# Optimization experiments

Measured on AMD Instinct MI355X. Metric: run time of the kernel, lower is better.

The kernel has to match this reference:

```python
import jax, jax.numpy as jnp
import numpy as np
from jax import lax

DW_THR = 4.0
PW_THR = 1e-3
EPS = 1e-5


def _bn(x, gamma, beta, mean, var):
    # inference-mode BatchNorm2d over channel axis 1
    inv = gamma * lax.rsqrt(var + EPS)
    return x * inv[None, :, None, None] + (beta - mean * inv)[None, :, None, None]


def _prune(x, thr):
    # zero each (batch, channel) feature map whose max-abs < thr
    maxabs = jnp.max(jnp.abs(x), axis=(2, 3), keepdims=True)  # [B,C,1,1]
    return jnp.where(maxabs < thr, jnp.zeros((), x.dtype), x)


def setup_inputs() -> dict:
    key = jax.random.key(0)
    ks = jax.random.split(key, 8)
    B, Cin, Cout, H, W = 32, 256, 512, 56, 56
    x = jax.random.normal(ks[0], (B, Cin, H, W), jnp.float32)
    dw_w = jax.random.normal(ks[1], (Cin, 1, 3, 3), jnp.float32) * (1.0 / 3.0)
    dw_b = jax.random.normal(ks[2], (Cin,), jnp.float32) * 0.1
    bn1_gamma = jnp.ones((Cin,), jnp.float32)
    bn1_beta = jnp.zeros((Cin,), jnp.float32)
    bn1_mean = jnp.zeros((Cin,), jnp.float32)
    bn1_var = jnp.ones((Cin,), jnp.float32)
    pw_w = jax.random.normal(ks[3], (Cout, Cin), jnp.float32) * (1.0 / np.sqrt(Cin))
    pw_b = jax.random.normal(ks[4], (Cout,), jnp.float32) * 0.1
    bn2_gamma = jnp.ones((Cout,), jnp.float32)
    bn2_beta = jnp.zeros((Cout,), jnp.float32)
    bn2_mean = jnp.zeros((Cout,), jnp.float32)
    bn2_var = jnp.ones((Cout,), jnp.float32)
    return dict(x=x, dw_w=dw_w, dw_b=dw_b,
                bn1_gamma=bn1_gamma, bn1_beta=bn1_beta, bn1_mean=bn1_mean, bn1_var=bn1_var,
                pw_w=pw_w, pw_b=pw_b,
                bn2_gamma=bn2_gamma, bn2_beta=bn2_beta, bn2_mean=bn2_mean, bn2_var=bn2_var)


def reference(x, dw_w, dw_b, bn1_gamma, bn1_beta, bn1_mean, bn1_var,
              pw_w, pw_b, bn2_gamma, bn2_beta, bn2_mean, bn2_var):
    Cin = x.shape[1]
    # depthwise 3x3 conv, padding=1, groups=Cin
    y = lax.conv_general_dilated(
        x, dw_w, window_strides=(1, 1), padding=((1, 1), (1, 1)),
        feature_group_count=Cin,
        dimension_numbers=('NCHW', 'OIHW', 'NCHW'))
    y = y + dw_b[None, :, None, None]
    y = jax.nn.relu(_bn(y, bn1_gamma, bn1_beta, bn1_mean, bn1_var))
    y = _prune(y, DW_THR)
    # pointwise 1x1 conv == channel GEMM
    z = jnp.einsum('bchw,oc->bohw', y, pw_w) + pw_b[None, :, None, None]
    z = jax.nn.relu(_bn(z, bn2_gamma, bn2_beta, bn2_mean, bn2_var))
    z = _prune(z, PW_THR)
    return z
```

## Files before the change

kernel.cpp:

```cpp
#include <hip/hip_runtime.h>
#include <hip/hip_bf16.h>

#define EPSV 1e-5f
#define DW_THR 4.0f
#define PW_THR 1e-3f

static constexpr int BB = 32, CIN = 256, COUT = 512, HH = 56, WW = 56, HW = HH * WW;

typedef __attribute__((ext_vector_type(8))) short bf16x8;
typedef __attribute__((ext_vector_type(4))) float f32x4;
typedef __attribute__((ext_vector_type(8))) unsigned short u16x8;

__device__ __forceinline__ void glds16(const void* g, void* l) {
    __builtin_amdgcn_global_load_lds((const __attribute__((address_space(1))) void*)g,
                                     (__attribute__((address_space(3))) void*)l, 16, 0, 0);
}

__global__ __launch_bounds__(256) void dwfold_kernel(
    const float* __restrict__ x, const float* __restrict__ dw_w, const float* __restrict__ dw_b,
    const float* __restrict__ g1, const float* __restrict__ b1,
    const float* __restrict__ m1, const float* __restrict__ v1,
    const float* __restrict__ pw_w, const float* __restrict__ pw_b,
    const float* __restrict__ g2, const float* __restrict__ b2,
    const float* __restrict__ m2, const float* __restrict__ v2,
    __hip_bfloat16* __restrict__ y, int* __restrict__ flags,
    __hip_bfloat16* __restrict__ Wf, float* __restrict__ cterm)
{
    __shared__ float xs[58 * 68];
    __shared__ float redw[4];
    const int tid = threadIdx.x;

    if (blockIdx.x < COUT) {
        const int o = blockIdx.x;
        const float inv = g2[o] * rsqrtf(v2[o] + EPSV);
        Wf[o * CIN + tid] = __float2bfloat16(pw_w[o * CIN + tid] * inv);
        if (tid == 0) cterm[o] = (pw_b[o] - m2[o]) * inv + b2[o];
        return;
    }

    const int blk = blockIdx.x - COUT;
    const int c   = blk & (CIN - 1);

    if (tid < 228) {
        int idx;
        if (tid < 58)       idx = 3 + tid;
        else if (tid < 116) idx = 57 * 68 + 3 + (tid - 58);
        else if (tid < 172) idx = (tid - 116 + 1) * 68 + 3;
        else                idx = (tid - 172 + 1) * 68 + 60;
        xs[idx] = 0.f;
    }
    const float* xp = x + (size_t)blk * HW;
    for (int i = tid; i < 56 * 14; i += 256) {
        int r = i / 14, q = i - r * 14;
        *(f32x4*)&xs[(r + 1) * 68 + 4 + q * 4] = *(const f32x4*)(xp + i * 4);
    }

    float w[9];
#pragma unroll
    for (int k = 0; k < 9; k++) w[k] = dw_w[c * 9 + k];
    const float inv = g1[c] * rsqrtf(v1[c] + EPSV);
    const float sh  = (dw_b[c] - m1[c]) * inv + b1[c];
    __syncthreads();

    float vals[14];
    float mx = 0.f;
    const int row = tid >> 2, strip = tid & 3;
    if (tid < 224) {
        const float* base = xs + row * 68 + strip * 14 + 4;
        float a0 = base[-1],       a1 = base[0];
        float b0 = base[68 - 1],   b1v = base[68];
        float c0 = base[136 - 1],  c1 = base[136];
#pragma unroll
        for (int i = 0; i < 14; i++) {
            const float a2 = base[i + 1];
            const float b2v = base[68 + i + 1];
            const float c2 = base[136 + i + 1];
            float s;
            s = a0 * w[0];
            s = fmaf(a1, w[1], s); s = fmaf(a2, w[2], s);
            s = fmaf(b0, w[3], s); s = fmaf(b1v, w[4], s); s = fmaf(b2v, w[5], s);
            s = fmaf(c0, w[6], s); s = fmaf(c1, w[7], s); s = fmaf(c2, w[8], s);
            const float val = fmaxf(fmaf(s, inv, sh), 0.f);
            vals[i] = val;
            mx = fmaxf(mx, val);
            a0 = a1; a1 = a2; b0 = b1v; b1v = b2v; c0 = c1; c1 = c2;
        }
    }

    for (int off = 32; off > 0; off >>= 1) mx = fmaxf(mx, __shfl_xor(mx, off));
    if ((tid & 63) == 0) redw[tid >> 6] = mx;
    __syncthreads();
    const float bmax = fmaxf(fmaxf(redw[0], redw[1]), fmaxf(redw[2], redw[3]));
    const int survive = (bmax >= DW_THR) ? 1 : 0;
    if (tid == 0) flags[blk] = survive;
    if (survive && tid < 224) {
        unsigned short* yp = (unsigned short*)(y + (size_t)blk * HW) + row * 56 + strip * 14;
#pragma unroll
        for (int i = 0; i < 7; i++) {
            ushort2 pk;
            pk.x = __bfloat16_as_ushort(__float2bfloat16(vals[2 * i]));
            pk.y = __bfloat16_as_ushort(__float2bfloat16(vals[2 * i + 1]));
            *(ushort2*)(yp + 2 * i) = pk;
        }
    }
}

__global__ __launch_bounds__(256) void gemm_kernel(
    const __hip_bfloat16* __restrict__ Wf_, const __hip_bfloat16* __restrict__ y_,
    const int* __restrict__ flags, const float* __restrict__ cterm,
    float* __restrict__ out, float* __restrict__ pmax)
{
    const int orig = blockIdx.x;
    const int blk  = (orig & 7) * 400 + (orig >> 3);
    const int b    = blk / 100;
    const int rem  = blk % 100;
    const int mt = rem / 25, nt = rem % 25;
    const int tid = threadIdx.x, l = tid & 63, wid = tid >> 6;
    const int wm = wid >> 1, wn = wid & 1;
    const int lr = l & 15, lk = l >> 4;
    const int o0 = mt * 128, n0 = nt * 128;

    __shared__ unsigned short Al[128 * 32];
    __shared__ unsigned short Bl[128 * 34];
    __shared__ int fl[CIN];

    fl[tid] = flags[b * CIN + tid];

    const short* W = (const short*)Wf_;
    const unsigned short* Y = (const unsigned short*)y_ + (size_t)b * CIN * HW;

    const int kch   = (((l & 3) ^ ((l >> 3) & 3)) << 3);
    const int rowA  = o0 + 32 * wid + (l >> 2);
    const short* asrc0 = W + (size_t)rowA * CIN + kch;
    const short* asrc1 = W + (size_t)(rowA + 16) * CIN + kch;

    const int cp = tid & 15, ng = tid >> 4;
    const int nB = n0 + ng * 8;
    const int nloc = ng * 8;

    f32x4 acc[4][4];
#pragma unroll
    for (int nr = 0; nr < 4; nr++)
#pragma unroll
        for (int mr = 0; mr < 4; mr++) acc[nr][mr] = (f32x4){0.f, 0.f, 0.f, 0.f};

    __syncthreads();

#pragma unroll
    for (int t = 0; t < 8; t++) {
        const int k0 = t * 32;
        glds16(asrc0 + k0, (void*)(&Al[(2 * wid) * 512]));
        glds16(asrc1 + k0, (void*)(&Al[(2 * wid + 1) * 512]));

        const int c0 = k0 + cp * 2;
        u16x8 v0 = (u16x8){0,0,0,0,0,0,0,0}, v1 = (u16x8){0,0,0,0,0,0,0,0};
        if (fl[c0])     v0 = *(const u16x8*)(Y + (size_t)c0 * HW + nB);
        if (fl[c0 + 1]) v1 = *(const u16x8*)(Y + (size_t)(c0 + 1) * HW + nB);
#pragma unroll
        for (int j = 0; j < 8; j++) {
            const unsigned pk = (unsigned)v0[j] | ((unsigned)v1[j] << 16);
            *(unsigned*)((char*)Bl + (nloc + j) * 68 + cp * 4) = pk;
        }
        __syncthreads();

        bf16x8 a[4], bb[4];
#pragma unroll
        for (int mr = 0; mr < 4; mr++) {
            const int r = wm * 64 + mr * 16 + lr;
            a[mr] = *(const bf16x8*)((const char*)Al + r * 64 + ((lk ^ ((r >> 1) & 3)) << 4));
        }
#pragma unroll
        for (int nr = 0; nr < 4; nr++) {
            const int r = wn * 64 + nr * 16 + lr;
            bb[nr] = *(const bf16x8*)((const char*)Bl + r * 68 + lk * 16);
        }
#pragma unroll
        for (int nr = 0; nr < 4; nr++)
#pragma unroll
            for (int mr = 0; mr < 4; mr++)
                acc[nr][mr] = __builtin_amdgcn_mfma_f32_16x16x32_bf16(bb[nr], a[mr], acc[nr][mr], 0, 0, 0);
        __syncthreads();
    }

    float ct[4], om[4];
#pragma unroll
    for (int mr = 0; mr < 4; mr++) {
        ct[mr] = cterm[o0 + wm * 64 + mr * 16 + lr];
        om[mr] = 0.f;
    }
    const int nb0 = n0 + wn * 64;
#pragma unroll
    for (int nr = 0; nr < 4; nr++) {
        const int n4 = nb0 + nr * 16 + lk * 4;
        if (n4 < HW) {
#pragma unroll
            for (int mr = 0; mr < 4; mr++) {
                const int o = o0 + wm * 64 + mr * 16 + lr;
                f32x4 z;
                z[0] = fmaxf(acc[nr][mr][0] + ct[mr], 0.f);
                z[1] = fmaxf(acc[nr][mr][1] + ct[mr], 0.f);
                z[2] = fmaxf(acc[nr][mr][2] + ct[mr], 0.f);
                z[3] = fmaxf(acc[nr][mr][3] + ct[mr], 0.f);
                __builtin_nontemporal_store(z, (f32x4*)(out + ((size_t)b * COUT + o) * HW + n4));
                om[mr] = fmaxf(om[mr], fmaxf(fmaxf(z[0], z[1]), fmaxf(z[2], z[3])));
            }
        }
    }
#pragma unroll
    for (int mr = 0; mr < 4; mr++) {
        om[mr] = fmaxf(om[mr], __shfl_xor(om[mr], 16));
        om[mr] = fmaxf(om[mr], __shfl_xor(om[mr], 32));
    }
    if (l < 16) {
#pragma unroll
        for (int mr = 0; mr < 4; mr++) {
            const int o = o0 + wm * 64 + mr * 16 + lr;
            pmax[(size_t)(b * COUT + o) * 50 + nt * 2 + wn] = om[mr];
        }
    }
}

__global__ __launch_bounds__(256) void fixup_kernel(const float* __restrict__ pmax, float* __restrict__ out)
{
    const int tid = threadIdx.x;
    const int blk = blockIdx.x * 4 + (tid >> 6);
    const int b = blk >> 9, o = blk & 511;
    const int lane = tid & 63;
    float m = (lane < 50) ? pmax[(size_t)(b * COUT + o) * 50 + lane] : 0.f;
#pragma unroll
    for (int d = 1; d < 64; d <<= 1) m = fmaxf(m, __shfl_xor(m, d));
    if (m < PW_THR) {
        float* p = out + ((size_t)b * COUT + o) * HW;
        for (int n = lane; n < HW; n += 64) p[n] = 0.f;
    }
}

extern "C" void kernel_launch(void* const* d_in, const int* in_sizes, int n_in,
                              void* d_out, int out_size, void* d_ws, size_t ws_size,
                              hipStream_t stream)
{
    const float* x    = (const float*)d_in[0];
    const float* dw_w = (const float*)d_in[1];
    const float* dw_b = (const float*)d_in[2];
    const float* g1   = (const float*)d_in[3];
    const float* b1   = (const float*)d_in[4];
    const float* m1   = (const float*)d_in[5];
    const float* v1   = (const float*)d_in[6];
    const float* pw_w = (const float*)d_in[7];
    const float* pw_b = (const float*)d_in[8];
    const float* g2   = (const float*)d_in[9];
    const float* b2   = (const float*)d_in[10];
    const float* m2   = (const float*)d_in[11];
    const float* v2   = (const float*)d_in[12];
    float* out = (float*)d_out;

    char* ws = (char*)d_ws;
    size_t off = 0;
    __hip_bfloat16* y  = (__hip_bfloat16*)(ws + off); off += (size_t)BB * CIN * HW * 2 + 256;
    int*   flags = (int*)(ws + off);   off += (size_t)BB * CIN * 4;
    __hip_bfloat16* Wf = (__hip_bfloat16*)(ws + off); off += (size_t)COUT * CIN * 2;
    float* cterm = (float*)(ws + off); off += (size_t)COUT * 4;
    float* pmax  = (float*)(ws + off); off += (size_t)BB * COUT * 50 * 4;

    dwfold_kernel<<<COUT + BB * CIN, 256, 0, stream>>>(
        x, dw_w, dw_b, g1, b1, m1, v1, pw_w, pw_b, g2, b2, m2, v2, y, flags, Wf, cterm);
    gemm_kernel<<<BB * 4 * 25, 256, 0, stream>>>(Wf, y, flags, cterm, out, pmax);
    fixup_kernel<<<BB * COUT / 4, 256, 0, stream>>>(pmax, out);
}
```

Before: 101.8 us.

## Widen depthwise per-thread strips with vector LDS loads; keep GEMM flags in registers

The depthwise kernel now has 112 threads each compute 28 outputs of a row, reading each input row as nine float4 LDS loads and writing bf16 results as 8-byte stores, instead of 224 threads doing 14 scalar-loaded outputs. This cuts LDS load instructions and store count but halves the active threads per block and raises register use. The GEMM kernel no longer stages per-channel prune flags in shared memory. Each thread packs the flags it needs into two bitmasks read from global memory, which removes the initial __syncthreads.

```diff
diff --git a/kernel.cpp b/kernel.cpp
--- a/kernel.cpp
+++ b/kernel.cpp
@@ -62,28 +62,33 @@
     const float sh  = (dw_b[c] - m1[c]) * inv + b1[c];
     __syncthreads();
 
-    float vals[14];
+    float part[28];
     float mx = 0.f;
-    const int row = tid >> 2, strip = tid & 3;
-    if (tid < 224) {
-        const float* base = xs + row * 68 + strip * 14 + 4;
-        float a0 = base[-1],       a1 = base[0];
-        float b0 = base[68 - 1],   b1v = base[68];
-        float c0 = base[136 - 1],  c1 = base[136];
-#pragma unroll
-        for (int i = 0; i < 14; i++) {
-            const float a2 = base[i + 1];
-            const float b2v = base[68 + i + 1];
-            const float c2 = base[136 + i + 1];
-            float s;
-            s = a0 * w[0];
-            s = fmaf(a1, w[1], s); s = fmaf(a2, w[2], s);
-            s = fmaf(b0, w[3], s); s = fmaf(b1v, w[4], s); s = fmaf(b2v, w[5], s);
-            s = fmaf(c0, w[6], s); s = fmaf(c1, w[7], s); s = fmaf(c2, w[8], s);
-            const float val = fmaxf(fmaf(s, inv, sh), 0.f);
-            vals[i] = val;
-            mx = fmaxf(mx, val);
-            a0 = a1; a1 = a2; b0 = b1v; b1v = b2v; c0 = c1; c1 = c2;
+    const int row = tid >> 1, strip = tid & 1;
+    if (tid < 112) {
+#pragma unroll
+        for (int i = 0; i < 28; i++) part[i] = 0.f;
+        const float* rbase = xs + row * 68 + strip * 28;
+#pragma unroll
+        for (int dr = 0; dr < 3; dr++) {
+            f32x4 f[9];
+#pragma unroll
+            for (int j = 0; j < 9; j++) f[j] = *(const f32x4*)(rbase + dr * 68 + j * 4);
+            const float w0 = w[dr * 3], w1 = w[dr * 3 + 1], w2 = w[dr * 3 + 2];
+#pragma unroll
+            for (int i = 0; i < 28; i++) {
+                const float e0 = f[(i + 3) >> 2][(i + 3) & 3];
+                const float e1 = f[(i + 4) >> 2][(i + 4) & 3];
+                const float e2 = f[(i + 5) >> 2][(i + 5) & 3];
+                part[i] = fmaf(e0, w0, part[i]);
+                part[i] = fmaf(e1, w1, part[i]);
+                part[i] = fmaf(e2, w2, part[i]);
+            }
+        }
+#pragma unroll
+        for (int i = 0; i < 28; i++) {
+            part[i] = fmaxf(fmaf(part[i], inv, sh), 0.f);
+            mx = fmaxf(mx, part[i]);
         }
     }
 
@@ -93,14 +98,16 @@
     const float bmax = fmaxf(fmaxf(redw[0], redw[1]), fmaxf(redw[2], redw[3]));
     const int survive = (bmax >= DW_THR) ? 1 : 0;
     if (tid == 0) flags[blk] = survive;
-    if (survive && tid < 224) {
-        unsigned short* yp = (unsigned short*)(y + (size_t)blk * HW) + row * 56 + strip * 14;
-#pragma unroll
-        for (int i = 0; i < 7; i++) {
-            ushort2 pk;
-            pk.x = __bfloat16_as_ushort(__float2bfloat16(vals[2 * i]));
-            pk.y = __bfloat16_as_ushort(__float2bfloat16(vals[2 * i + 1]));
-            *(ushort2*)(yp + 2 * i) = pk;
+    if (survive && tid < 112) {
+        unsigned short* yp = (unsigned short*)(y + (size_t)blk * HW) + row * 56 + strip * 28;
+#pragma unroll
+        for (int q = 0; q < 7; q++) {
+            ushort4 pk;
+            pk.x = __bfloat16_as_ushort(__float2bfloat16(part[4 * q]));
+            pk.y = __bfloat16_as_ushort(__float2bfloat16(part[4 * q + 1]));
+            pk.z = __bfloat16_as_ushort(__float2bfloat16(part[4 * q + 2]));
+            pk.w = __bfloat16_as_ushort(__float2bfloat16(part[4 * q + 3]));
+            *(ushort4*)(yp + 4 * q) = pk;
         }
     }
 }
@@ -122,9 +129,6 @@
 
     __shared__ unsigned short Al[128 * 32];
     __shared__ unsigned short Bl[128 * 34];
-    __shared__ int fl[CIN];
-
-    fl[tid] = flags[b * CIN + tid];
 
     const short* W = (const short*)Wf_;
     const unsigned short* Y = (const unsigned short*)y_ + (size_t)b * CIN * HW;
@@ -138,13 +142,19 @@
     const int nB = n0 + ng * 8;
     const int nloc = ng * 8;
 
+    const int* flg = flags + b * CIN + cp * 2;
+    unsigned fm0 = 0, fm1 = 0;
+#pragma unroll
+    for (int t = 0; t < 8; t++) {
+        fm0 |= (flg[t * 32]     ? 1u : 0u) << t;
+        fm1 |= (flg[t * 32 + 1] ? 1u : 0u) << t;
+    }
+
     f32x4 acc[4][4];
 #pragma unroll
     for (int nr = 0; nr < 4; nr++)
 #pragma unroll
         for (int mr = 0; mr < 4; mr++) acc[nr][mr] = (f32x4){0.f, 0.f, 0.f, 0.f};
-
-    __syncthreads();
 
 #pragma unroll
     for (int t = 0; t < 8; t++) {
@@ -154,8 +164,8 @@
 
         const int c0 = k0 + cp * 2;
         u16x8 v0 = (u16x8){0,0,0,0,0,0,0,0}, v1 = (u16x8){0,0,0,0,0,0,0,0};
-        if (fl[c0])     v0 = *(const u16x8*)(Y + (size_t)c0 * HW + nB);
-        if (fl[c0 + 1]) v1 = *(const u16x8*)(Y + (size_t)(c0 + 1) * HW + nB);
+        if ((fm0 >> t) & 1) v0 = *(const u16x8*)(Y + (size_t)c0 * HW + nB);
+        if ((fm1 >> t) & 1) v1 = *(const u16x8*)(Y + (size_t)(c0 + 1) * HW + nB);
 #pragma unroll
         for (int j = 0; j < 8; j++) {
             const unsigned pk = (unsigned)v0[j] | ((unsigned)v1[j] << 16);
```

Result: slower. 106.3 us (+4.5%).
